# Kernel optimization log

Measured on AMD Instinct MI355X. Metric: run time of the kernel, lower is better.

## Reference

```python
import jax, jax.numpy as jnp
import numpy as np

WBITS = 4
ABITS = 8
OBITS = 8


def fwht(x):
    """Normalized fast Walsh-Hadamard transform along the last axis (n power of 2).
    Equivalent to matmul_hadU with had_K = I, K = 1 (n = 4096 = 2^12)."""
    shape = x.shape
    n = shape[-1]
    x = x.reshape(-1, n)
    h = 1
    while h < n:
        x = x.reshape(-1, n // (2 * h), 2, h)
        a, b = x[:, :, 0, :], x[:, :, 1, :]
        x = jnp.concatenate([a + b, a - b], axis=-1).reshape(-1, n)
        h *= 2
    inv_sqrt_n = jnp.asarray(1.0 / np.sqrt(n), x.dtype)
    return (x * inv_sqrt_n).reshape(shape)


def sym_fake_quant(t, bits, axis):
    """Symmetric min-max RTN fake quantization (per-channel for weights,
    per-token for activations)."""
    qmax = jnp.asarray(2.0 ** (bits - 1) - 1.0, t.dtype)
    scale = jnp.max(jnp.abs(t), axis=axis, keepdims=True) / qmax
    scale = jnp.maximum(scale, jnp.asarray(1e-8, t.dtype))
    q = jnp.clip(jnp.round(t / scale), -qmax, qmax)
    return q * scale


def setup_inputs() -> dict:
    key = jax.random.key(0)
    k1, k2, k3 = jax.random.split(key, 3)
    B, S, DIN, DOUT = 4, 2048, 4096, 4096
    return {
        "input": jax.random.normal(k1, (B, S, DIN), dtype=jnp.float32),
        "weight": jax.random.normal(k2, (DOUT, DIN), dtype=jnp.float32) * 0.02,
        "bias": jax.random.normal(k3, (DOUT,), dtype=jnp.float32) * 0.01,
    }


def reference(input, weight, bias):
    # online full Hadamard rotation of activations
    x = fwht(input)
    # activation quant (per-token, symmetric int8 fake-quant)
    x = sym_fake_quant(x, ABITS, axis=-1)
    # weight quant (per-output-channel, symmetric int4 fake-quant)
    w = sym_fake_quant(weight, WBITS, axis=-1)
    # F.linear: x @ w.T + b
    out = jnp.einsum("bsi,oi->bso", x, w) + bias
    # output quant (per-token, symmetric int8 fake-quant)
    out = sym_fake_quant(out, OBITS, axis=-1)
    return out
```

## Files before the change

### kernel.cpp

```cpp
#include <hip/hip_runtime.h>
#include <hip/hip_bf16.h>

#define DIN 4096
#define DOUT 4096
#define NROWS 8192

typedef int i32x4 __attribute__((ext_vector_type(4)));

__device__ __forceinline__ float block_absmax(float m, float* red) {
  #pragma unroll
  for (int off = 32; off > 0; off >>= 1)
    m = fmaxf(m, __shfl_down(m, off));
  const int tid = threadIdx.x;
  if ((tid & 63) == 0) red[tid >> 6] = m;
  __syncthreads();
  return fmaxf(fmaxf(red[0], red[1]), fmaxf(red[2], red[3]));
}

__global__ __launch_bounds__(256) void fused_quant_kernel(
    const float* __restrict__ in, const float* __restrict__ w,
    char* __restrict__ qx, char* __restrict__ qw,
    float* __restrict__ sx, float* __restrict__ sw) {
  __shared__ float lds[4352];
  __shared__ float red[4];
  const int tid = threadIdx.x;

  if (blockIdx.x < NROWS) {
    const size_t row = blockIdx.x;
    const int th = tid >> 4, tl = tid & 15;
    float v[16];
    const float4* src = (const float4*)(in + row * DIN);
    #pragma unroll
    for (int k = 0; k < 4; ++k) {
      float4 f = src[tid * 4 + k];
      v[4 * k + 0] = f.x; v[4 * k + 1] = f.y;
      v[4 * k + 2] = f.z; v[4 * k + 3] = f.w;
    }
    #pragma unroll
    for (int hb = 1; hb < 16; hb <<= 1)
      #pragma unroll
      for (int j = 0; j < 16; ++j)
        if (!(j & hb)) {
          float a0 = v[j], b0 = v[j | hb];
          v[j] = a0 + b0; v[j | hb] = a0 - b0;
        }
    #pragma unroll
    for (int j = 0; j < 16; ++j) lds[17 * tid + j] = v[j];
    __syncthreads();
    #pragma unroll
    for (int j = 0; j < 16; ++j) v[j] = lds[272 * th + 17 * j + tl];
    #pragma unroll
    for (int hb = 1; hb < 16; hb <<= 1)
      #pragma unroll
      for (int j = 0; j < 16; ++j)
        if (!(j & hb)) {
          float a0 = v[j], b0 = v[j | hb];
          v[j] = a0 + b0; v[j | hb] = a0 - b0;
        }
    #pragma unroll
    for (int j = 0; j < 16; ++j) lds[272 * th + 17 * j + tl] = v[j];
    __syncthreads();
    #pragma unroll
    for (int j = 0; j < 16; ++j) v[j] = lds[272 * j + 17 * th + tl];
    #pragma unroll
    for (int hb = 1; hb < 16; hb <<= 1)
      #pragma unroll
      for (int j = 0; j < 16; ++j)
        if (!(j & hb)) {
          float a0 = v[j], b0 = v[j | hb];
          v[j] = a0 + b0; v[j | hb] = a0 - b0;
        }
    float m = 0.0f;
    #pragma unroll
    for (int j = 0; j < 16; ++j) m = fmaxf(m, fabsf(v[j]));
    #pragma unroll
    for (int j = 0; j < 16; ++j) lds[272 * j + 17 * th + tl] = v[j];
    float mx = block_absmax(m, red) * 0.015625f;
    float scale = fmaxf(mx / 127.0f, 1e-8f);
    if (tid == 0) sx[row] = scale;
    const float rs = 1.0f / scale;
    char pk[16];
    #pragma unroll
    for (int j = 0; j < 16; ++j) {
      float q = fminf(fmaxf(rintf((lds[17 * tid + j] * 0.015625f) * rs), -127.f),
                      127.f);
      pk[j] = (char)q;
    }
    *(int4*)(qx + row * DIN + (size_t)tid * 16) = *(const int4*)pk;
  } else {
    const size_t row = blockIdx.x - NROWS;
    const float4* src = (const float4*)(w + row * DIN);
    float4* b4 = (float4*)lds;
    float m = 0.0f;
    for (int i = tid; i < DIN / 4; i += 256) {
      float4 v = src[i];
      b4[i] = v;
      m = fmaxf(m, fmaxf(fmaxf(fabsf(v.x), fabsf(v.y)),
                         fmaxf(fabsf(v.z), fabsf(v.w))));
    }
    float mx = block_absmax(m, red);
    float scale = fmaxf(mx / 7.0f, 1e-8f);
    if (tid == 0) sw[row] = scale;
    char* dst = qw + row * DIN;
    const float rs = 1.0f / scale;
    for (int i0 = tid * 4; i0 < DIN; i0 += 1024) {
      char4 pk;
      float q0 = fminf(fmaxf(rintf(lds[i0 + 0] * rs), -7.f), 7.f);
      float q1 = fminf(fmaxf(rintf(lds[i0 + 1] * rs), -7.f), 7.f);
      float q2 = fminf(fmaxf(rintf(lds[i0 + 2] * rs), -7.f), 7.f);
      float q3 = fminf(fmaxf(rintf(lds[i0 + 3] * rs), -7.f), 7.f);
      pk.x = (char)q0; pk.y = (char)q1; pk.z = (char)q2; pk.w = (char)q3;
      *(char4*)(dst + i0) = pk;
    }
  }
}

__global__ __launch_bounds__(512, 2) void gemm_kernel(
    const char* __restrict__ A,
    const char* __restrict__ Bt,
    const float* __restrict__ sx, const float* __restrict__ sw,
    const float* __restrict__ bias, float* __restrict__ out) {
  __shared__ char lds[131072];
  const int tid = threadIdx.x;
  const int lane = tid & 63;
  const int wid = tid >> 6;
  const int wr = wid >> 2;
  const int wc = wid & 3;
  int bid = blockIdx.x;
  int swz = (bid & 7) * 32 + (bid >> 3);
  const size_t rowA = (size_t)(swz >> 4) * 512;
  const size_t col0 = (size_t)(swz & 15) * 256;
  const int slot0 = (((lane >> 4) ^ (lane & 7)) << 4);

  i32x4 acc[4][2][4] = {};
  i32x4 fb[4][2];
  i32x4 fa[2][2];

#define STAGE(MAT, GROW0, KT, LBASE)                                          \
  {                                                                           \
    _Pragma("unroll")                                                         \
    for (int j = 0; j < 2; ++j) {                                             \
      int chunk = j * 8 + wid;                                                \
      int rr = chunk * 8 + (lane >> 3);                                       \
      int cc = ((KT) & 31) * 128 + (((lane & 7) ^ (lane >> 3)) << 4);         \
      const char* src = (MAT) + ((GROW0) + rr) * (size_t)DIN + cc;            \
      __builtin_amdgcn_global_load_lds(                                       \
          (const __attribute__((address_space(1))) void*)src,                 \
          (__attribute__((address_space(3))) void*)(lds + (LBASE) +           \
                                                    chunk * 1024),            \
          16, 0, 0);                                                          \
    }                                                                         \
  }
#define STAGE_A(P, HALF, KT)                                                  \
  STAGE(A, rowA + (((KT) >= 32) ? 256 : 0) + (HALF) * 128, KT,                \
        (P) * 32768 + (HALF) * 16384)
#define STAGE_B(P, HALF, KT) \
  STAGE(Bt, col0 + (HALF) * 128, KT, 65536 + (P) * 32768 + (HALF) * 16384)

#define DS_A(Q, P)                                                            \
  {                                                                           \
    _Pragma("unroll")                                                         \
    for (int mm = 0; mm < 2; ++mm) {                                          \
      int ar = (Q) * 64 + wr * 32 + mm * 16 + (lane & 15);                    \
      _Pragma("unroll")                                                       \
      for (int kk = 0; kk < 2; ++kk)                                          \
        fa[mm][kk] =                                                          \
            *(const i32x4*)(lds + (P) * 32768 + ar * 128 + (slot0 ^ (kk * 64))); \
    }                                                                         \
  }
#define DS_B(P)                                                               \
  {                                                                           \
    _Pragma("unroll")                                                         \
    for (int nn = 0; nn < 4; ++nn) {                                          \
      int br = wc * 64 + nn * 16 + (lane & 15);                               \
      _Pragma("unroll")                                                       \
      for (int kk = 0; kk < 2; ++kk)                                          \
        fb[nn][kk] = *(const i32x4*)(lds + 65536 + (P) * 32768 + br * 128 +   \
                                     (slot0 ^ (kk * 64)));                    \
    }                                                                         \
  }
#define MFMA16(Q)                                                             \
  {                                                                           \
    __builtin_amdgcn_s_setprio(1);                                            \
    _Pragma("unroll")                                                         \
    for (int kk = 0; kk < 2; ++kk)                                            \
      _Pragma("unroll")                                                       \
      for (int mm = 0; mm < 2; ++mm)                                          \
        _Pragma("unroll")                                                     \
        for (int nn = 0; nn < 4; ++nn)                                        \
          acc[Q][mm][nn] = __builtin_amdgcn_mfma_i32_16x16x64_i8(             \
              fb[nn][kk], fa[mm][kk], acc[Q][mm][nn], 0, 0, 0);               \
    __builtin_amdgcn_s_setprio(0);                                            \
  }
#define BAR() __builtin_amdgcn_s_barrier()
#define WAIT_LGKM0() asm volatile("s_waitcnt lgkmcnt(0)" ::: "memory")

#define EPI(T)                                                                \
  {                                                                           \
    _Pragma("unroll")                                                         \
    for (int q = 0; q < 4; ++q) {                                             \
      _Pragma("unroll")                                                       \
      for (int mm = 0; mm < 2; ++mm) {                                        \
        size_t gr = rowA + (T) * 256 + q * 64 + wr * 32 + mm * 16 + (lane & 15); \
        float sxr = sx[gr];                                                   \
        float* orow = out + gr * DOUT;                                        \
        _Pragma("unroll")                                                     \
        for (int nn = 0; nn < 4; ++nn) {                                      \
          size_t gc0 = col0 + wc * 64 + nn * 16 + ((lane >> 4) << 2);         \
          float4 swv = *(const float4*)(sw + gc0);                            \
          float4 bv = *(const float4*)(bias + gc0);                           \
          float4 o;                                                           \
          o.x = (float)acc[q][mm][nn][0] * (sxr * swv.x) + bv.x;              \
          o.y = (float)acc[q][mm][nn][1] * (sxr * swv.y) + bv.y;              \
          o.z = (float)acc[q][mm][nn][2] * (sxr * swv.z) + bv.z;              \
          o.w = (float)acc[q][mm][nn][3] * (sxr * swv.w) + bv.w;              \
          *(float4*)(orow + gc0) = o;                                         \
        }                                                                     \
      }                                                                       \
    }                                                                         \
  }

  STAGE_B(0, 0, 0); STAGE_B(0, 1, 0); STAGE_A(0, 0, 0); STAGE_A(0, 1, 0);
  STAGE_B(1, 0, 1); STAGE_B(1, 1, 1); STAGE_A(1, 0, 1);
  asm volatile("s_waitcnt vmcnt(6)" ::: "memory");
  BAR();

  #pragma unroll 1
  for (int i = 0; i < 32; ++i) {
    const int a = 2 * i, b = 2 * i + 1;
    const bool nl = (i < 31);
    if (i == 16) {
      EPI(0);
      #pragma unroll
      for (int q = 0; q < 4; ++q)
        #pragma unroll
        for (int mm = 0; mm < 2; ++mm)
          #pragma unroll
          for (int nn = 0; nn < 4; ++nn)
            acc[q][mm][nn] = (i32x4){0, 0, 0, 0};
      asm volatile("s_waitcnt vmcnt(0)" ::: "memory");
    }
    DS_A(0, 0); DS_B(0);
    STAGE_A(1, 1, b);
    asm volatile("s_waitcnt lgkmcnt(8)" ::: "memory");
    BAR(); WAIT_LGKM0();
    MFMA16(0);
    BAR();
    DS_A(1, 0);
    if (nl) STAGE_B(0, 0, a + 2);
    BAR(); WAIT_LGKM0();
    MFMA16(1);
    BAR();
    DS_A(2, 0);
    if (nl) STAGE_B(0, 1, a + 2);
    BAR(); WAIT_LGKM0();
    MFMA16(2);
    BAR();
    DS_A(3, 0);
    if (nl) STAGE_A(0, 0, a + 2);
    BAR(); WAIT_LGKM0();
    MFMA16(3);
    if (nl) { asm volatile("s_waitcnt vmcnt(6)" ::: "memory"); }
    else    { asm volatile("s_waitcnt vmcnt(0)" ::: "memory"); }
    BAR();
    DS_A(0, 1); DS_B(1);
    if (nl) STAGE_A(0, 1, a + 2);
    asm volatile("s_waitcnt lgkmcnt(8)" ::: "memory");
    BAR(); WAIT_LGKM0();
    MFMA16(0);
    BAR();
    DS_A(1, 1);
    if (nl) STAGE_B(1, 0, b + 2);
    BAR(); WAIT_LGKM0();
    MFMA16(1);
    BAR();
    DS_A(2, 1);
    if (nl) STAGE_B(1, 1, b + 2);
    BAR(); WAIT_LGKM0();
    MFMA16(2);
    BAR();
    DS_A(3, 1);
    if (nl) STAGE_A(1, 0, b + 2);
    BAR(); WAIT_LGKM0();
    MFMA16(3);
    if (nl) { asm volatile("s_waitcnt vmcnt(6)" ::: "memory"); }
    BAR();
  }

  EPI(1);
#undef STAGE
#undef STAGE_A
#undef STAGE_B
#undef DS_A
#undef DS_B
#undef MFMA16
#undef BAR
#undef WAIT_LGKM0
#undef EPI
}

__global__ __launch_bounds__(256) void rowquant_kernel(float* __restrict__ out) {
  __shared__ float red[4];
  const int tid = threadIdx.x;
  const size_t row = blockIdx.x;
  float4* g4 = (float4*)(out + row * DOUT);
  float4 v[4];
  float m = 0.0f;
  #pragma unroll
  for (int k = 0; k < 4; ++k) {
    v[k] = g4[tid + k * 256];
    m = fmaxf(m, fmaxf(fmaxf(fabsf(v[k].x), fabsf(v[k].y)),
                       fmaxf(fabsf(v[k].z), fabsf(v[k].w))));
  }
  float mx = block_absmax(m, red);
  float scale = fmaxf(mx / 127.0f, 1e-8f);
  #pragma unroll
  for (int k = 0; k < 4; ++k) {
    float4 w = v[k];
    w.x = fminf(fmaxf(rintf(w.x / scale), -127.0f), 127.0f) * scale;
    w.y = fminf(fmaxf(rintf(w.y / scale), -127.0f), 127.0f) * scale;
    w.z = fminf(fmaxf(rintf(w.z / scale), -127.0f), 127.0f) * scale;
    w.w = fminf(fmaxf(rintf(w.w / scale), -127.0f), 127.0f) * scale;
    g4[tid + k * 256] = w;
  }
}

extern "C" void kernel_launch(void* const* d_in, const int* in_sizes, int n_in,
                              void* d_out, int out_size, void* d_ws, size_t ws_size,
                              hipStream_t stream) {
  (void)in_sizes; (void)n_in; (void)out_size; (void)ws_size;
  const float* input = (const float*)d_in[0];
  const float* weight = (const float*)d_in[1];
  const float* bias = (const float*)d_in[2];
  float* out = (float*)d_out;
  char* ws = (char*)d_ws;
  char* qx = ws;
  char* qw = ws + ((size_t)32 << 20);
  float* sx = (float*)(ws + ((size_t)48 << 20));
  float* sw = (float*)(ws + ((size_t)48 << 20) + ((size_t)32 << 10));

  fused_quant_kernel<<<NROWS + DOUT, 256, 0, stream>>>(input, weight, qx, qw,
                                                       sx, sw);
  gemm_kernel<<<256, 512, 0, stream>>>(qx, qw, sx, sw, bias, out);
  rowquant_kernel<<<NROWS, 256, 0, stream>>>(out);
}
```

Measured before the change: 229.5 us.

## Shrink GEMM tile to 256x128 with K=64 stages for higher occupancy

Replaces the 512x256-output-per-block int8 GEMM (128KB LDS, 256 blocks, K-tile 128) with 256x128 tiles, K-tile 64, 48KB LDS and 1024 blocks at up to 4 blocks per CU. Each wave now holds a smaller accumulator set and issues 4 MFMAs per sub-step, with a new XOR swizzle for the 64-byte LDS rows. The intent is more resident blocks and better latency hiding than a single large block per CU. The cost is lower operand reuse per loaded byte, more barriers per MFMA, and a scalar, less coalesced epilogue store pattern.

```diff
diff --git a/kernel.cpp b/kernel.cpp
--- a/kernel.cpp
+++ b/kernel.cpp
@@ -115,188 +115,142 @@
   }
 }
 
-__global__ __launch_bounds__(512, 2) void gemm_kernel(
+__global__ __launch_bounds__(512, 4) void gemm_kernel(
     const char* __restrict__ A,
     const char* __restrict__ Bt,
     const float* __restrict__ sx, const float* __restrict__ sw,
     const float* __restrict__ bias, float* __restrict__ out) {
-  __shared__ char lds[131072];
+  __shared__ char lds[49152];
   const int tid = threadIdx.x;
   const int lane = tid & 63;
   const int wid = tid >> 6;
-  const int wr = wid >> 2;
-  const int wc = wid & 3;
+  const int wr = wid >> 1;
+  const int wc = wid & 1;
   int bid = blockIdx.x;
-  int swz = (bid & 7) * 32 + (bid >> 3);
-  const size_t rowA = (size_t)(swz >> 4) * 512;
-  const size_t col0 = (size_t)(swz & 15) * 256;
-  const int slot0 = (((lane >> 4) ^ (lane & 7)) << 4);
-
-  i32x4 acc[4][2][4] = {};
-  i32x4 fb[4][2];
-  i32x4 fa[2][2];
-
-#define STAGE(MAT, GROW0, KT, LBASE)                                          \
+  int swz = (bid & 7) * 128 + (bid >> 3);
+  const size_t row0 = (size_t)(swz >> 5) * 256;
+  const size_t col0 = (size_t)(swz & 31) * 128;
+  const int g16 = lane >> 4;
+
+  i32x4 acc[4][4] = {};
+  i32x4 fb[4];
+  i32x4 fa;
+
+#define STAGE_UNIT(MAT, GROW0, KT, LBASE)                                     \
   {                                                                           \
-    _Pragma("unroll")                                                         \
-    for (int j = 0; j < 2; ++j) {                                             \
-      int chunk = j * 8 + wid;                                                \
-      int rr = chunk * 8 + (lane >> 3);                                       \
-      int cc = ((KT) & 31) * 128 + (((lane & 7) ^ (lane >> 3)) << 4);         \
-      const char* src = (MAT) + ((GROW0) + rr) * (size_t)DIN + cc;            \
-      __builtin_amdgcn_global_load_lds(                                       \
-          (const __attribute__((address_space(1))) void*)src,                 \
-          (__attribute__((address_space(3))) void*)(lds + (LBASE) +           \
-                                                    chunk * 1024),            \
-          16, 0, 0);                                                          \
-    }                                                                         \
-  }
-#define STAGE_A(P, HALF, KT)                                                  \
-  STAGE(A, rowA + (((KT) >= 32) ? 256 : 0) + (HALF) * 128, KT,                \
-        (P) * 32768 + (HALF) * 16384)
-#define STAGE_B(P, HALF, KT) \
-  STAGE(Bt, col0 + (HALF) * 128, KT, 65536 + (P) * 32768 + (HALF) * 16384)
-
-#define DS_A(Q, P)                                                            \
+    int rr = wid * 16 + (lane >> 2);                                          \
+    int cc = (KT) * 64 + ((((lane & 3) ^ ((rr >> 1) & 3))) << 4);             \
+    const char* src = (MAT) + ((GROW0) + rr) * (size_t)DIN + cc;              \
+    __builtin_amdgcn_global_load_lds(                                         \
+        (const __attribute__((address_space(1))) void*)src,                   \
+        (__attribute__((address_space(3))) void*)(lds + (LBASE) +             \
+                                                  wid * 1024),                \
+        16, 0, 0);                                                            \
+  }
+#define STAGE_A(P, HALF, KT) \
+  STAGE_UNIT(A, row0 + (HALF) * 128, KT, (P) * 16384 + (HALF) * 8192)
+#define STAGE_B(P, KT) STAGE_UNIT(Bt, col0, KT, 32768 + (P) * 8192)
+
+#define DS_FA(Q, P)                                                           \
   {                                                                           \
-    _Pragma("unroll")                                                         \
-    for (int mm = 0; mm < 2; ++mm) {                                          \
-      int ar = (Q) * 64 + wr * 32 + mm * 16 + (lane & 15);                    \
-      _Pragma("unroll")                                                       \
-      for (int kk = 0; kk < 2; ++kk)                                          \
-        fa[mm][kk] =                                                          \
-            *(const i32x4*)(lds + (P) * 32768 + ar * 128 + (slot0 ^ (kk * 64))); \
-    }                                                                         \
-  }
-#define DS_B(P)                                                               \
+    int ar = (Q) * 64 + wr * 16 + (lane & 15);                                \
+    fa = *(const i32x4*)(lds + (P) * 16384 + ar * 64 +                        \
+                         ((g16 ^ ((ar >> 1) & 3)) << 4));                     \
+  }
+#define DS_FB(P)                                                              \
   {                                                                           \
     _Pragma("unroll")                                                         \
     for (int nn = 0; nn < 4; ++nn) {                                          \
       int br = wc * 64 + nn * 16 + (lane & 15);                               \
-      _Pragma("unroll")                                                       \
-      for (int kk = 0; kk < 2; ++kk)                                          \
-        fb[nn][kk] = *(const i32x4*)(lds + 65536 + (P) * 32768 + br * 128 +   \
-                                     (slot0 ^ (kk * 64)));                    \
+      fb[nn] = *(const i32x4*)(lds + 32768 + (P) * 8192 + br * 64 +           \
+                               ((g16 ^ ((br >> 1) & 3)) << 4));               \
     }                                                                         \
   }
-#define MFMA16(Q)                                                             \
+#define MFMA4(Q)                                                              \
   {                                                                           \
     __builtin_amdgcn_s_setprio(1);                                            \
     _Pragma("unroll")                                                         \
-    for (int kk = 0; kk < 2; ++kk)                                            \
-      _Pragma("unroll")                                                       \
-      for (int mm = 0; mm < 2; ++mm)                                          \
-        _Pragma("unroll")                                                     \
-        for (int nn = 0; nn < 4; ++nn)                                        \
-          acc[Q][mm][nn] = __builtin_amdgcn_mfma_i32_16x16x64_i8(             \
-              fb[nn][kk], fa[mm][kk], acc[Q][mm][nn], 0, 0, 0);               \
+    for (int nn = 0; nn < 4; ++nn)                                            \
+      acc[Q][nn] = __builtin_amdgcn_mfma_i32_16x16x64_i8(                     \
+          fa, fb[nn], acc[Q][nn], 0, 0, 0);                                   \
     __builtin_amdgcn_s_setprio(0);                                            \
   }
 #define BAR() __builtin_amdgcn_s_barrier()
 #define WAIT_LGKM0() asm volatile("s_waitcnt lgkmcnt(0)" ::: "memory")
 
-#define EPI(T)                                                                \
-  {                                                                           \
-    _Pragma("unroll")                                                         \
-    for (int q = 0; q < 4; ++q) {                                             \
-      _Pragma("unroll")                                                       \
-      for (int mm = 0; mm < 2; ++mm) {                                        \
-        size_t gr = rowA + (T) * 256 + q * 64 + wr * 32 + mm * 16 + (lane & 15); \
-        float sxr = sx[gr];                                                   \
-        float* orow = out + gr * DOUT;                                        \
-        _Pragma("unroll")                                                     \
-        for (int nn = 0; nn < 4; ++nn) {                                      \
-          size_t gc0 = col0 + wc * 64 + nn * 16 + ((lane >> 4) << 2);         \
-          float4 swv = *(const float4*)(sw + gc0);                            \
-          float4 bv = *(const float4*)(bias + gc0);                           \
-          float4 o;                                                           \
-          o.x = (float)acc[q][mm][nn][0] * (sxr * swv.x) + bv.x;              \
-          o.y = (float)acc[q][mm][nn][1] * (sxr * swv.y) + bv.y;              \
-          o.z = (float)acc[q][mm][nn][2] * (sxr * swv.z) + bv.z;              \
-          o.w = (float)acc[q][mm][nn][3] * (sxr * swv.w) + bv.w;              \
-          *(float4*)(orow + gc0) = o;                                         \
-        }                                                                     \
-      }                                                                       \
-    }                                                                         \
-  }
-
-  STAGE_B(0, 0, 0); STAGE_B(0, 1, 0); STAGE_A(0, 0, 0); STAGE_A(0, 1, 0);
-  STAGE_B(1, 0, 1); STAGE_B(1, 1, 1); STAGE_A(1, 0, 1);
-  asm volatile("s_waitcnt vmcnt(6)" ::: "memory");
+  STAGE_B(0, 0); STAGE_A(0, 0, 0); STAGE_A(0, 1, 0);
+  STAGE_B(1, 1); STAGE_A(1, 0, 1);
+  asm volatile("s_waitcnt vmcnt(2)" ::: "memory");
   BAR();
 
   #pragma unroll 1
   for (int i = 0; i < 32; ++i) {
     const int a = 2 * i, b = 2 * i + 1;
     const bool nl = (i < 31);
-    if (i == 16) {
-      EPI(0);
+    DS_FA(0, 0); DS_FB(0);
+    STAGE_A(1, 1, b);
+    BAR(); WAIT_LGKM0();
+    MFMA4(0);
+    BAR();
+    DS_FA(1, 0);
+    if (nl) STAGE_B(0, a + 2);
+    BAR(); WAIT_LGKM0();
+    MFMA4(1);
+    BAR();
+    DS_FA(2, 0);
+    if (nl) STAGE_A(0, 0, a + 2);
+    BAR(); WAIT_LGKM0();
+    MFMA4(2);
+    BAR();
+    DS_FA(3, 0);
+    BAR(); WAIT_LGKM0();
+    MFMA4(3);
+    if (nl) { asm volatile("s_waitcnt vmcnt(2)" ::: "memory"); }
+    else    { asm volatile("s_waitcnt vmcnt(0)" ::: "memory"); }
+    BAR();
+    DS_FA(0, 1); DS_FB(1);
+    if (nl) STAGE_A(0, 1, a + 2);
+    BAR(); WAIT_LGKM0();
+    MFMA4(0);
+    BAR();
+    DS_FA(1, 1);
+    if (nl) STAGE_B(1, b + 2);
+    BAR(); WAIT_LGKM0();
+    MFMA4(1);
+    BAR();
+    DS_FA(2, 1);
+    if (nl) STAGE_A(1, 0, b + 2);
+    BAR(); WAIT_LGKM0();
+    MFMA4(2);
+    BAR();
+    DS_FA(3, 1);
+    BAR(); WAIT_LGKM0();
+    MFMA4(3);
+    if (nl) { asm volatile("s_waitcnt vmcnt(2)" ::: "memory"); }
+    BAR();
+  }
+
+  #pragma unroll
+  for (int q = 0; q < 4; ++q) {
+    #pragma unroll
+    for (int nn = 0; nn < 4; ++nn) {
+      size_t gc = col0 + wc * 64 + nn * 16 + (lane & 15);
+      float swc = sw[gc], bc = bias[gc];
       #pragma unroll
-      for (int q = 0; q < 4; ++q)
-        #pragma unroll
-        for (int mm = 0; mm < 2; ++mm)
-          #pragma unroll
-          for (int nn = 0; nn < 4; ++nn)
-            acc[q][mm][nn] = (i32x4){0, 0, 0, 0};
-      asm volatile("s_waitcnt vmcnt(0)" ::: "memory");
-    }
-    DS_A(0, 0); DS_B(0);
-    STAGE_A(1, 1, b);
-    asm volatile("s_waitcnt lgkmcnt(8)" ::: "memory");
-    BAR(); WAIT_LGKM0();
-    MFMA16(0);
-    BAR();
-    DS_A(1, 0);
-    if (nl) STAGE_B(0, 0, a + 2);
-    BAR(); WAIT_LGKM0();
-    MFMA16(1);
-    BAR();
-    DS_A(2, 0);
-    if (nl) STAGE_B(0, 1, a + 2);
-    BAR(); WAIT_LGKM0();
-    MFMA16(2);
-    BAR();
-    DS_A(3, 0);
-    if (nl) STAGE_A(0, 0, a + 2);
-    BAR(); WAIT_LGKM0();
-    MFMA16(3);
-    if (nl) { asm volatile("s_waitcnt vmcnt(6)" ::: "memory"); }
-    else    { asm volatile("s_waitcnt vmcnt(0)" ::: "memory"); }
-    BAR();
-    DS_A(0, 1); DS_B(1);
-    if (nl) STAGE_A(0, 1, a + 2);
-    asm volatile("s_waitcnt lgkmcnt(8)" ::: "memory");
-    BAR(); WAIT_LGKM0();
-    MFMA16(0);
-    BAR();
-    DS_A(1, 1);
-    if (nl) STAGE_B(1, 0, b + 2);
-    BAR(); WAIT_LGKM0();
-    MFMA16(1);
-    BAR();
-    DS_A(2, 1);
-    if (nl) STAGE_B(1, 1, b + 2);
-    BAR(); WAIT_LGKM0();
-    MFMA16(2);
-    BAR();
-    DS_A(3, 1);
-    if (nl) STAGE_A(1, 0, b + 2);
-    BAR(); WAIT_LGKM0();
-    MFMA16(3);
-    if (nl) { asm volatile("s_waitcnt vmcnt(6)" ::: "memory"); }
-    BAR();
-  }
-
-  EPI(1);
-#undef STAGE
+      for (int j = 0; j < 4; ++j) {
+        size_t gr = row0 + q * 64 + wr * 16 + (g16 << 2) + j;
+        out[gr * DOUT + gc] = (float)acc[q][nn][j] * (sx[gr] * swc) + bc;
+      }
+    }
+  }
+#undef STAGE_UNIT
 #undef STAGE_A
 #undef STAGE_B
-#undef DS_A
-#undef DS_B
-#undef MFMA16
+#undef DS_FA
+#undef DS_FB
+#undef MFMA4
 #undef BAR
 #undef WAIT_LGKM0
-#undef EPI
 }
 
 __global__ __launch_bounds__(256) void rowquant_kernel(float* __restrict__ out) {
@@ -341,6 +295,6 @@
 
   fused_quant_kernel<<<NROWS + DOUT, 256, 0, stream>>>(input, weight, qx, qw,
                                                        sx, sw);
-  gemm_kernel<<<256, 512, 0, stream>>>(qx, qw, sx, sw, bias, out);
+  gemm_kernel<<<1024, 512, 0, stream>>>(qx, qw, sx, sw, bias, out);
   rowquant_kernel<<<NROWS, 256, 0, stream>>>(out);
 }
```

After: 239.9 us. 4.6% more time.
